# Performance work log

Measured on AMD Instinct MI355X. Metric: run time of the kernel, lower is better.

Reference implementation:

```python
import jax, jax.numpy as jnp
import numpy as np

C = 256      # d_model
H = 8        # nhead
DF = 1024    # dim_feedforward
LE = 2048    # ego tokens
LA = 2048    # other-agent tokens
N_MATCH = 1024


def setup_inputs() -> dict:
    key = jax.random.key(0)
    ks = jax.random.split(key, 16)
    def rn(k, shape, s=0.02):
        return jax.random.normal(k, shape, dtype=jnp.float32) * s
    inp = {}
    inp['x_ego'] = jax.random.normal(ks[0], (LE, C), dtype=jnp.float32)
    inp['x_agent'] = jax.random.normal(ks[1], (LA, C), dtype=jnp.float32)
    # query_fusion MLP(2C -> C -> C -> C), torch Linear weight is (out, in)
    inp['Wf1'] = rn(ks[2], (C, 2 * C)); inp['bf1'] = jnp.zeros((C,), jnp.float32)
    inp['Wf2'] = rn(ks[3], (C, C));     inp['bf2'] = jnp.zeros((C,), jnp.float32)
    inp['Wf3'] = rn(ks[4], (C, C));     inp['bf3'] = jnp.zeros((C,), jnp.float32)
    # nn.MultiheadAttention packed in-proj and out-proj
    inp['Wqkv'] = rn(ks[5], (3 * C, C)); inp['bqkv'] = jnp.zeros((3 * C,), jnp.float32)
    inp['Wo'] = rn(ks[6], (C, C));       inp['bo'] = jnp.zeros((C,), jnp.float32)
    # FFN
    inp['W1'] = rn(ks[7], (DF, C)); inp['b1'] = jnp.zeros((DF,), jnp.float32)
    inp['W2'] = rn(ks[8], (C, DF)); inp['b2'] = jnp.zeros((C,), jnp.float32)
    # LayerNorms
    inp['g1'] = jnp.ones((C,), jnp.float32); inp['be1'] = jnp.zeros((C,), jnp.float32)
    inp['g2'] = jnp.ones((C,), jnp.float32); inp['be2'] = jnp.zeros((C,), jnp.float32)
    # unique 1D positions: first N_MATCH agent positions overlap ego, rest don't
    inp['pos_ego'] = jnp.arange(LE, dtype=jnp.int32)
    pa = np.concatenate([np.arange(N_MATCH), np.arange(LA - N_MATCH) + 10_000_000])
    inp['pos_agent'] = jnp.asarray(pa, dtype=jnp.int32)
    inp['n_remain'] = LA - N_MATCH  # static python int
    return inp


def _ln(t, g, b):
    m = t.mean(-1, keepdims=True)
    v = t.var(-1, keepdims=True)
    return (t - m) / jnp.sqrt(v + 1e-5) * g + b


def reference(x_ego, x_agent, Wf1, bf1, Wf2, bf2, Wf3, bf3, Wqkv, bqkv, Wo, bo,
              W1, b1, W2, b2, g1, be1, g2, be2, pos_ego, pos_agent, n_remain):
    # ---- position-keyed grouping / fuse (replaces the host-side dict loop) ----
    eq = pos_agent[:, None] == pos_ego[None, :]          # [La, Le]
    matched_e = eq.any(axis=0)                           # ego token has same-pos agent token
    agent_for_ego = jnp.argmax(eq, axis=0)               # [Le] matching agent index (valid where matched)
    fused_in = jnp.concatenate([x_ego, x_agent[agent_for_ego]], axis=-1)  # [Le, 2C]
    h = jax.nn.relu(fused_in @ Wf1.T + bf1)
    h = jax.nn.relu(h @ Wf2.T + bf2)
    fused = h @ Wf3.T + bf3                              # query_fusion MLP output [Le, C]
    ego_out = jnp.where(matched_e[:, None], fused, x_ego)
    # agent tokens with no ego match, in original agent order (fixed count n_remain)
    remain_idx = jnp.nonzero(~eq.any(axis=1), size=n_remain)[0]
    q = jnp.concatenate([ego_out, x_agent[remain_idx]], axis=0)[None]  # (1, Lq, C)
    kv = jnp.concatenate([x_ego, x_agent], axis=0)[None]               # (1, Lk, C)
    # ---- MultiheadAttention (batch_first, eval: dropout off) ----
    Wq, Wk, Wv = jnp.split(Wqkv, 3, axis=0)
    bq, bk, bv = jnp.split(bqkv, 3, axis=0)
    dh = C // H
    def heads(t, W, b):
        return (t @ W.T + b).reshape(1, -1, H, dh).transpose(0, 2, 1, 3)
    qh, kh, vh = heads(q, Wq, bq), heads(kv, Wk, bk), heads(kv, Wv, bv)
    scores = jnp.einsum('bhqd,bhkd->bhqk', qh, kh) / (float(dh) ** 0.5)
    attn = jax.nn.softmax(scores, axis=-1)
    o = jnp.einsum('bhqk,bhkd->bhqd', attn, vh).transpose(0, 2, 1, 3).reshape(1, -1, C)
    o = o @ Wo.T + bo
    # ---- residual + norm1 + FFN + residual + norm2 ----
    yq = _ln(q + o, g1, be1)
    ff = jax.nn.relu(yq @ W1.T + b1) @ W2.T + b2
    return _ln(yq + ff, g2, be2)
```

## Files before the change

### kernel.cpp

```cpp
#include <hip/hip_runtime.h>


#define LE 2048
#define LA 2048
#define CDIM 256
#define HN 8
#define DH 32
#define DFF 1024
#define NREM 1024
#define LQC 3072
#define LKC 4096
#define KSPLIT 8
#define NIT (LKC / KSPLIT / 64)

typedef unsigned short u16;
typedef unsigned int u32;
typedef __attribute__((ext_vector_type(8))) short bf16x8;
typedef __attribute__((ext_vector_type(8))) _Float16 f16x8;
typedef __attribute__((ext_vector_type(4))) float f32x4;

#define MFMA __builtin_amdgcn_mfma_f32_16x16x32_bf16

__device__ __forceinline__ u32 pk_bf16(float a, float b) {
    u32 ua = (__builtin_bit_cast(u32, a) + 0x8000u) >> 16;
    u32 ub = (__builtin_bit_cast(u32, b) + 0x8000u) >> 16;
    return ua | (ub << 16);
}
__device__ __forceinline__ u16 bf16_1(float a) {
    return (u16)((__builtin_bit_cast(u32, a) + 0x8000u) >> 16);
}
__device__ __forceinline__ float fast_exp2(float x) {
    return __builtin_amdgcn_exp2f(x);
}
__device__ __forceinline__ bf16x8 ld_pack8(const float* p) {
    float4 f0 = *(const float4*)p;
    float4 f1 = *(const float4*)(p + 4);
    union { u32 u[4]; bf16x8 v; } o;
    o.u[0] = pk_bf16(f0.x, f0.y); o.u[1] = pk_bf16(f0.z, f0.w);
    o.u[2] = pk_bf16(f1.x, f1.y); o.u[3] = pk_bf16(f1.z, f1.w);
    return o.v;
}

struct WPtrs { const float* p[7]; };
__constant__ __device__ const int woff[8] = {0, 131072, 196608, 262144,
                                             458752, 524288, 786432, 1048576};

__global__ __launch_bounds__(1024) void k_prep(const int* __restrict__ pos_ego,
                                               const int* __restrict__ pos_agent,
                                               int* __restrict__ afe,
                                               int* __restrict__ matched,
                                               int* __restrict__ remain,
                                               const float* __restrict__ x_ego,
                                               const float* __restrict__ x_agent,
                                               WPtrs wp, u16* __restrict__ wb,
                                               u16* __restrict__ kv_b) {
    const int b = blockIdx.x;
    const int t = threadIdx.x;
    if (b == 0) {
        __shared__ int keyA[4096], valA[4096], keyE[4096];
        __shared__ int unm[2048];
#pragma unroll
        for (int i = 0; i < 4; ++i) { keyA[t + i * 1024] = -1; keyE[t + i * 1024] = -1; }
        __syncthreads();
#pragma unroll
        for (int i = 0; i < 2; ++i) {
            int a = t + i * 1024;
            int p = pos_agent[a];
            u32 h = ((u32)p * 2654435761u) >> 20;
            while (true) {
                int prev = atomicCAS(&keyA[h], -1, p);
                if (prev == -1) { valA[h] = a; break; }
                h = (h + 1) & 4095;
            }
// ... 43 lines not shown
            __syncthreads();
            valA[t] += v;
            __syncthreads();
        }
        int pos = valA[t] - cnt;
        if (f0 && pos < NREM) remain[pos] = 2 * t;
        if (f1 && pos + f0 < NREM) remain[pos + f0] = 2 * t + 1;
    } else if (b <= 128) {
        int g = ((b - 1) * 1024 + t) * 8;
        int s = 0;
#pragma unroll
        for (int i = 1; i < 7; ++i) s += (g >= woff[i]);
        const float* src = wp.p[s] + (g - woff[s]);
        float4 f0 = *(const float4*)(src);
        float4 f1 = *(const float4*)(src + 4);
        uint4 o;
        o.x = pk_bf16(f0.x, f0.y); o.y = pk_bf16(f0.z, f0.w);
        o.z = pk_bf16(f1.x, f1.y); o.w = pk_bf16(f1.z, f1.w);
        *(uint4*)(wb + g) = o;
    } else {
        int tt = (b - 129) * 1024 + t;
        int j = tt >> 5, c8 = tt & 31;
        const float* src = (j < LE) ? (x_ego + (size_t)j * CDIM)
                                    : (x_agent + (size_t)(j - LE) * CDIM);
        float4 f0 = *(const float4*)(src + c8 * 8);
        float4 f1 = *(const float4*)(src + c8 * 8 + 4);
        uint4 o;
        o.x = pk_bf16(f0.x, f0.y); o.y = pk_bf16(f0.z, f0.w);
        o.z = pk_bf16(f1.x, f1.y); o.w = pk_bf16(f1.z, f1.w);
        *(uint4*)(kv_b + (size_t)j * CDIM + c8 * 8) = o;
    }
}

__global__ __launch_bounds__(256) void k_fmlp(const float* __restrict__ x_ego,
                                              const float* __restrict__ x_agent,
                                              const int* __restrict__ afe,
                                              const int* __restrict__ matched,
                                              const int* __restrict__ remain,
                                              const u16* __restrict__ Wf1_b,
                                              const u16* __restrict__ Wf2_b,
                                              const u16* __restrict__ Wf3_b,
                                              const float* __restrict__ bf1,
                                              const float* __restrict__ bf2,
                                              const float* __restrict__ bf3,
                                              float* __restrict__ qbuf,
                                              u16* __restrict__ qbuf_b) {
    const int blk = blockIdx.x;
    const int tid = threadIdx.x;
    if (blk >= 128) {
        int rb = (blk - 128) * 64 + (tid >> 2);
        int row = LE + rb;
        int col = (tid & 3) * 64;
        int idx = remain[rb];
        idx = min(max(idx, 0), LA - 1);
        const float* src = x_agent + (size_t)idx * CDIM + col;
        float* dq = qbuf + (size_t)row * CDIM + col;
        u16* db = qbuf_b + (size_t)row * CDIM + col;
#pragma unroll
        for (int i = 0; i < 16; ++i) {
            float4 v = *(const float4*)(src + i * 4);
            *(float4*)(dq + i * 4) = v;
            *(uint2*)(db + i * 4) = make_uint2(pk_bf16(v.x, v.y), pk_bf16(v.z, v.w));
        }
        return;
    }
    __shared__ u16 h1[16 * 256];
    __shared__ u16 h2[16 * 256];
    const int w = tid >> 6, lane = tid & 63, quad = lane >> 4, qi = lane & 15;
    const int R0 = blk * 16;
    const int rg = R0 + qi;
    {
        const float* pe = x_ego + (size_t)rg * CDIM + quad * 8;
        const float* pg = x_agent + (size_t)afe[rg] * CDIM + quad * 8;
        f32x4 acc[4] = {};
        const u16* pb = Wf1_b + (size_t)(w * 64 + qi) * 512 + quad * 8;
#pragma unroll
        for (int kk = 0; kk < 256; kk += 32) {
            bf16x8 a = ld_pack8(pe + kk);
#pragma unroll
            for (int j = 0; j < 4; ++j) {
                bf16x8 bfr = *(const bf16x8*)(pb + (size_t)j * 16 * 512 + kk);
                acc[j] = MFMA(a, bfr, acc[j], 0, 0, 0);
            }
        }
#pragma unroll
        for (int kk = 0; kk < 256; kk += 32) {
            bf16x8 a = ld_pack8(pg + kk);
#pragma unroll
            for (int j = 0; j < 4; ++j) {
                bf16x8 bfr = *(const bf16x8*)(pb + (size_t)j * 16 * 512 + 256 + kk);
                acc[j] = MFMA(a, bfr, acc[j], 0, 0, 0);
            }
        }
#pragma unroll
        for (int j = 0; j < 4; ++j) {
            int col = w * 64 + j * 16 + qi;
            float bs = bf1[col];
#pragma unroll
            for (int r = 0; r < 4; ++r) {
                int row = quad * 4 + r;
                float v = fmaxf(acc[j][r] + bs, 0.f);
                int byte = (row * 512 + col * 2) ^ ((row & 7) << 4);
                *(u16*)((char*)h1 + byte) = bf16_1(v);
            }
        }
    }
    __syncthreads();
    {
        f32x4 acc[4] = {};
        const u16* pb = Wf2_b + (size_t)(w * 64 + qi) * 256 + quad * 8;
#pragma unroll
        for (int kk = 0; kk < 256; kk += 32) {
            int byte = (qi * 512 + (kk + quad * 8) * 2) ^ ((qi & 7) << 4);
            bf16x8 a = *(const bf16x8*)((char*)h1 + byte);
#pragma unroll
            for (int j = 0; j < 4; ++j) {
                bf16x8 bfr = *(const bf16x8*)(pb + (size_t)j * 16 * 256 + kk);
                acc[j] = MFMA(a, bfr, acc[j], 0, 0, 0);
            }
        }
#pragma unroll
        for (int j = 0; j < 4; ++j) {
            int col = w * 64 + j * 16 + qi;
            float bs = bf2[col];
#pragma unroll
            for (int r = 0; r < 4; ++r) {
                int row = quad * 4 + r;
                float v = fmaxf(acc[j][r] + bs, 0.f);
                int byte = (row * 512 + col * 2) ^ ((row & 7) << 4);
                *(u16*)((char*)h2 + byte) = bf16_1(v);
            }
        }
    }
    __syncthreads();
    {
        f32x4 acc[4] = {};
        const u16* pb = Wf3_b + (size_t)(w * 64 + qi) * 256 + quad * 8;
#pragma unroll
        for (int kk = 0; kk < 256; kk += 32) {
            int byte = (qi * 512 + (kk + quad * 8) * 2) ^ ((qi & 7) << 4);
            bf16x8 a = *(const bf16x8*)((char*)h2 + byte);
#pragma unroll
            for (int j = 0; j < 4; ++j) {
                bf16x8 bfr = *(const bf16x8*)(pb + (size_t)j * 16 * 256 + kk);
                acc[j] = MFMA(a, bfr, acc[j], 0, 0, 0);
            }
        }
        int m[4];
#pragma unroll
        for (int r = 0; r < 4; ++r) m[r] = matched[R0 + quad * 4 + r];
#pragma unroll
        for (int j = 0; j < 4; ++j) {
            int col = w * 64 + j * 16 + qi;
            float bs = bf3[col];
#pragma unroll
            for (int r = 0; r < 4; ++r) {
                int row = R0 + quad * 4 + r;
                float v = acc[j][r] + bs;
                if (!m[r]) v = x_ego[(size_t)row * CDIM + col];
                qbuf[(size_t)row * CDIM + col] = v;
                qbuf_b[(size_t)row * CDIM + col] = bf16_1(v);
            }
        }
    }
}

__global__ __launch_bounds__(256) void k_qkv(const u16* __restrict__ qbuf_b,
                                             const u16* __restrict__ kv_b,
                                             const u16* __restrict__ Wq,
                                             const u16* __restrict__ Wkv,
                                             const float* __restrict__ bqkv,
                                             u16* __restrict__ qb,
                                             u16* __restrict__ kbp,
                                             u16* __restrict__ vtb,
                                             float qscale) {
    int b;
    {
        int p = blockIdx.x;
        int c = p & 7, s = p >> 3;
        b = c * 88 + s;
    }
    const u16 *A, *B;
    const float* bias;
    int bm, bn, mode;
    if (b < 192) {
        A = qbuf_b; B = Wq; bias = bqkv;
        bm = (b >> 2) * 64; bn = (b & 3) * 64; mode = 0;
    } else {
        int c = b - 192;
        A = kv_b; B = Wkv; bias = bqkv + 256;
        bm = (c >> 3) * 64; bn = (c & 7) * 64; mode = 1;
    }
    const int tid = threadIdx.x;
    const int w = tid >> 6, lane = tid & 63;
    const int quad = lane >> 4, qi = lane & 15;
    const int wm = w >> 1, wn = w & 1;
    const int K = 256;

    const u16* pa0 = A + (size_t)(bm + wm * 32 + qi) * K + quad * 8;
// ... 136 lines not shown
        bf16x8 pa0 = *(bf16x8*)&pb[rd0];
        bf16x8 pa1 = *(bf16x8*)&pb[rd1];

        bf16x8 v00 = *(const bf16x8*)&Vt[buf][v00o];
        bf16x8 v01 = *(const bf16x8*)&Vt[buf][v01o];
        bf16x8 v10 = *(const bf16x8*)&Vt[buf][v00o + 16 * 64];
        bf16x8 v11 = *(const bf16x8*)&Vt[buf][v01o + 16 * 64];
        O0 = MFMA(pa0, v00, O0, 0, 0, 0);
        O0 = MFMA(pa1, v01, O0, 0, 0, 0);
        O1 = MFMA(pa0, v10, O1, 0, 0, 0);
        O1 = MFMA(pa1, v11, O1, 0, 0, 0);

        if (more) {
            *(bf16x8*)&Kt[buf ^ 1][kdst] = knext;
            *(bf16x8*)&Vt[buf ^ 1][vdst] = vnext;
        }
        buf ^= 1;
    }

    lsum += __shfl_xor(lsum, 16, 64);
    lsum += __shfl_xor(lsum, 32, 64);

    int pbase = (h * KSPLIT + ks) * LQC + q0;
    if (quad == 0) Pl[pbase + qi] = lsum;
#pragma unroll
    for (int r = 0; r < 4; ++r) {
        int q = quad * 4 + r;
        u16* pa = Pacc + (size_t)(pbase + q) * 32;
        pa[qi] = __builtin_bit_cast(u16, (_Float16)O0[r]);
        pa[16 + qi] = __builtin_bit_cast(u16, (_Float16)O1[r]);
    }
}

__global__ __launch_bounds__(256) void k_oln(const float* __restrict__ Pl,
                                             const u16* __restrict__ Pacc,
                                             const u16* __restrict__ Wo_b,
                                             const float* __restrict__ bo,
                                             const float* __restrict__ qbuf,
                                             const float* __restrict__ g1,
                                             const float* __restrict__ be1,
                                             float* __restrict__ yq,
                                             u16* __restrict__ yq_b) {
    __shared__ u16 At[16 * 256];
    __shared__ float red[16][4][2];
    const int tid = threadIdx.x;
    const int R0 = blockIdx.x * 16;
    {
        int row = tid >> 4, cg = tid & 15;
        int h = cg >> 1, dh = (cg & 1) * 16;
        int r = R0 + row;
        float L = 0.f;
        float o[16] = {};
#pragma unroll
        for (int ks = 0; ks < 8; ++ks) {
            size_t pidx = (size_t)(h * 8 + ks) * LQC + r;
            L += Pl[pidx];
            const u16* pa = Pacc + pidx * 32 + dh;
            f16x8 v0 = *(const f16x8*)(pa);
            f16x8 v1 = *(const f16x8*)(pa + 8);
#pragma unroll
            for (int i = 0; i < 8; ++i) {
                o[i] += (float)v0[i];
                o[8 + i] += (float)v1[i];
            }
        }
        float invL = 1.0f / L;
        int cb = h * 32 + dh;
#pragma unroll
        for (int i = 0; i < 8; ++i) {
            int c0 = cb + 2 * i;
            u32 pk = pk_bf16(o[2 * i] * invL, o[2 * i + 1] * invL);
            int byte = (row * 512 + c0 * 2) ^ ((row & 7) << 4);
            *(u32*)((char*)At + byte) = pk;
        }
    }
    __syncthreads();
    const int w = tid >> 6, lane = tid & 63, quad = lane >> 4, qi = lane & 15;
    f32x4 acc[4] = {};
    const u16* pb = Wo_b + (size_t)(w * 64 + qi) * 256 + quad * 8;
#pragma unroll
    for (int kk = 0; kk < 256; kk += 32) {
        int byte = (qi * 512 + (kk + quad * 8) * 2) ^ ((qi & 7) << 4);
        bf16x8 a = *(const bf16x8*)((char*)At + byte);
#pragma unroll
        for (int j = 0; j < 4; ++j) {
            bf16x8 bfr = *(const bf16x8*)(pb + (size_t)j * 16 * 256 + kk);
            acc[j] = MFMA(a, bfr, acc[j], 0, 0, 0);
        }
    }
    float v[4][4], s[4] = {}, sq[4] = {};
#pragma unroll
    for (int j = 0; j < 4; ++j) {
        int col = w * 64 + j * 16 + qi;
        float bs = bo[col];
#pragma unroll
        for (int r = 0; r < 4; ++r) {
            int row = R0 + quad * 4 + r;
            float x = acc[j][r] + bs + qbuf[(size_t)row * CDIM + col];
            v[j][r] = x; s[r] += x; sq[r] += x * x;
        }
    }
#pragma unroll
    for (int off = 1; off < 16; off <<= 1) {
#pragma unroll
        for (int r = 0; r < 4; ++r) {
            s[r] += __shfl_xor(s[r], off, 64);
            sq[r] += __shfl_xor(sq[r], off, 64);
        }
    }
    if (qi == 0) {
#pragma unroll
        for (int r = 0; r < 4; ++r) {
            red[quad * 4 + r][w][0] = s[r];
            red[quad * 4 + r][w][1] = sq[r];
        }
    }
    __syncthreads();
    float mean[4], rstd[4];
#pragma unroll
    for (int r = 0; r < 4; ++r) {
        int rl = quad * 4 + r;
        float st = red[rl][0][0] + red[rl][1][0] + red[rl][2][0] + red[rl][3][0];
        float sqt = red[rl][0][1] + red[rl][1][1] + red[rl][2][1] + red[rl][3][1];
        mean[r] = st * (1.f / 256.f);
        float var = sqt * (1.f / 256.f) - mean[r] * mean[r];
        rstd[r] = rsqrtf(var + 1e-5f);
    }
#pragma unroll
    for (int j = 0; j < 4; ++j) {
        int col = w * 64 + j * 16 + qi;
        float gg = g1[col], bb = be1[col];
#pragma unroll
        for (int r = 0; r < 4; ++r) {
            int row = R0 + quad * 4 + r;
            float o = (v[j][r] - mean[r]) * rstd[r] * gg + bb;
            yq[(size_t)row * CDIM + col] = o;
            yq_b[(size_t)row * CDIM + col] = bf16_1(o);
        }
    }
}

__global__ __launch_bounds__(256) void k_ffn(const u16* __restrict__ yq_b,
                                             const float* __restrict__ yq,
                                             const u16* __restrict__ W1_b,
                                             const float* __restrict__ b1,
                                             const u16* __restrict__ W2_b,
                                             const float* __restrict__ b2,
                                             const float* __restrict__ g2,
                                             const float* __restrict__ be2,
                                             float* __restrict__ out) {
    __shared__ u16 hT[16 * 1024];
    __shared__ float red[16][4][2];
    const int tid = threadIdx.x;
    const int w = tid >> 6, lane = tid & 63, quad = lane >> 4, qi = lane & 15;
    const int R0 = blockIdx.x * 16;
    {
        const u16* pa = yq_b + (size_t)(R0 + qi) * 256 + quad * 8;
        f32x4 acc[16] = {};
        const u16* pb = W1_b + (size_t)(w * 256 + qi) * 256 + quad * 8;
#pragma unroll
        for (int kk = 0; kk < 256; kk += 32) {
            bf16x8 a = *(const bf16x8*)(pa + kk);
#pragma unroll
            for (int j = 0; j < 16; ++j) {
                bf16x8 bfr = *(const bf16x8*)(pb + (size_t)j * 16 * 256 + kk);
                acc[j] = MFMA(a, bfr, acc[j], 0, 0, 0);
            }
        }
#pragma unroll
        for (int j = 0; j < 16; ++j) {
            int col = w * 256 + j * 16 + qi;
            float bs = b1[col];
#pragma unroll
            for (int r = 0; r < 4; ++r) {
                int row = quad * 4 + r;
                float v = fmaxf(acc[j][r] + bs, 0.f);
                int byte = (row * 2048 + col * 2) ^ ((row & 7) << 4);
                *(u16*)((char*)hT + byte) = bf16_1(v);
            }
        }
    }
    __syncthreads();
    f32x4 acc[4] = {};
    const u16* pb = W2_b + (size_t)(w * 64 + qi) * 1024 + quad * 8;
#pragma unroll 4
    for (int kk = 0; kk < 1024; kk += 32) {
        int byte = (qi * 2048 + (kk + quad * 8) * 2) ^ ((qi & 7) << 4);
        bf16x8 a = *(const bf16x8*)((char*)hT + byte);
#pragma unroll
        for (int j = 0; j < 4; ++j) {
            bf16x8 bfr = *(const bf16x8*)(pb + (size_t)j * 16 * 1024 + kk);
            acc[j] = MFMA(a, bfr, acc[j], 0, 0, 0);
        }
    }
    float v[4][4], s[4] = {}, sq[4] = {};
#pragma unroll
    for (int j = 0; j < 4; ++j) {
        int col = w * 64 + j * 16 + qi;
        float bs = b2[col];
#pragma unroll
        for (int r = 0; r < 4; ++r) {
            int row = R0 + quad * 4 + r;
            float x = acc[j][r] + bs + yq[(size_t)row * CDIM + col];
            v[j][r] = x; s[r] += x; sq[r] += x * x;
        }
    }
#pragma unroll
    for (int off = 1; off < 16; off <<= 1) {
#pragma unroll
        for (int r = 0; r < 4; ++r) {
            s[r] += __shfl_xor(s[r], off, 64);
            sq[r] += __shfl_xor(sq[r], off, 64);
        }
    }
    if (qi == 0) {
#pragma unroll
        for (int r = 0; r < 4; ++r) {
            red[quad * 4 + r][w][0] = s[r];
            red[quad * 4 + r][w][1] = sq[r];
        }
    }
    __syncthreads();
    float mean[4], rstd[4];
#pragma unroll
    for (int r = 0; r < 4; ++r) {
        int rl = quad * 4 + r;
        float st = red[rl][0][0] + red[rl][1][0] + red[rl][2][0] + red[rl][3][0];
        float sqt = red[rl][0][1] + red[rl][1][1] + red[rl][2][1] + red[rl][3][1];
        mean[r] = st * (1.f / 256.f);
        float var = sqt * (1.f / 256.f) - mean[r] * mean[r];
        rstd[r] = rsqrtf(var + 1e-5f);
    }
#pragma unroll
    for (int j = 0; j < 4; ++j) {
        int col = w * 64 + j * 16 + qi;
        float gg = g2[col], bb = be2[col];
#pragma unroll
        for (int r = 0; r < 4; ++r) {
            int row = R0 + quad * 4 + r;
            out[(size_t)row * CDIM + col] = (v[j][r] - mean[r]) * rstd[r] * gg + bb;
        }
    }
}

extern "C" void kernel_launch(void* const* d_in, const int* in_sizes, int n_in,
                              void* d_out, int out_size, void* d_ws, size_t ws_size,
                              hipStream_t stream) {
    const float* x_ego = (const float*)d_in[0];
    const float* x_agent = (const float*)d_in[1];
    const float* Wf1 = (const float*)d_in[2];
    const float* bf1 = (const float*)d_in[3];
    const float* Wf2 = (const float*)d_in[4];
    const float* bf2 = (const float*)d_in[5];
    const float* Wf3 = (const float*)d_in[6];
    const float* bf3 = (const float*)d_in[7];
    const float* Wqkv = (const float*)d_in[8];
    const float* bqkv = (const float*)d_in[9];
    const float* Wo = (const float*)d_in[10];
    const float* bo = (const float*)d_in[11];
    const float* W1 = (const float*)d_in[12];
    const float* b1 = (const float*)d_in[13];
    const float* W2 = (const float*)d_in[14];
    const float* b2 = (const float*)d_in[15];
    const float* g1 = (const float*)d_in[16];
    const float* be1 = (const float*)d_in[17];
    const float* g2 = (const float*)d_in[18];
    const float* be2 = (const float*)d_in[19];
    const int* pos_ego = (const int*)d_in[20];
    const int* pos_agent = (const int*)d_in[21];

    float* ws = (float*)d_ws;
    size_t o = 0;
    float* qbuf = ws + o; o += 786432;
    float* yq = ws + o; o += 786432;
    float* Pl = ws + o; o += HN * KSPLIT * LQC;
    u16* Pacc = (u16*)(ws + o); o += (size_t)HN * KSPLIT * LQC * 16;
    u16* wb = (u16*)(ws + o); o += 524288;
    u16* qbuf_b = (u16*)(ws + o); o += 393216;
    u16* kv_b = (u16*)(ws + o); o += 524288;
    u16* qb = (u16*)(ws + o); o += 393216;
    u16* kb = (u16*)(ws + o); o += 524288;
    u16* vtb = (u16*)(ws + o); o += 524288;
    u16* yq_b = (u16*)(ws + o); o += 393216;
    int* afe = (int*)(ws + o);
    int* matched = afe + LE;
    int* remain = matched + LE;

    const u16* Wf1_b = wb + 0;
    const u16* Wf2_b = wb + 131072;
    const u16* Wf3_b = wb + 196608;
    const u16* Wq_b = wb + 262144;
    const u16* Wkv_b = wb + 327680;
    const u16* Wo_b = wb + 458752;
    const u16* W1_b = wb + 524288;
    const u16* W2_b = wb + 786432;

    WPtrs wp;
    wp.p[0] = Wf1; wp.p[1] = Wf2; wp.p[2] = Wf3; wp.p[3] = Wqkv;
    wp.p[4] = Wo; wp.p[5] = W1; wp.p[6] = W2;

    k_prep<<<257, 1024, 0, stream>>>(pos_ego, pos_agent, afe, matched, remain,
                                     x_ego, x_agent, wp, wb, kv_b);

    const float qscale = 0.17677669529663687f * 1.4426950408889634f;

    k_fmlp<<<144, 256, 0, stream>>>(x_ego, x_agent, afe, matched, remain,
                                    Wf1_b, Wf2_b, Wf3_b, bf1, bf2, bf3,
                                    qbuf, qbuf_b);

    k_qkv<<<704, 256, 0, stream>>>(qbuf_b, kv_b, Wq_b, Wkv_b, bqkv, qb, kb, vtb, qscale);

    attn_mfma<<<dim3(LQC / 64, HN, KSPLIT), 256, 0, stream>>>(qb, kb, vtb, Pl, Pacc);

    k_oln<<<LQC / 16, 256, 0, stream>>>(Pl, Pacc, Wo_b, bo, qbuf, g1, be1, yq, yq_b);

    k_ffn<<<LQC / 16, 256, 0, stream>>>(yq_b, yq, W1_b, b1, W2_b, b2, g2, be2,
                                        (float*)d_out);
}
```

Measured before the change: 223.0 us.

## Repartition row-wise MLP/LN kernels into 8-row, 1024-thread blocks

The fused-MLP, out-proj+LayerNorm and FFN kernels switch from 16-row blocks of 4 waves to 8-row blocks of 16 waves, each wave owning a narrower column slice. This doubles the grid and spreads the GEMM work over more waves so more CUs stay busy on these small-M stages. The cost is that half of each 16x16 MFMA tile is wasted, because only 8 rows are valid and rows are duplicated across quads, so weights are re-read by twice as many blocks. The LayerNorm reductions now combine partials from 16 waves.

```diff
diff --git a/kernel.cpp b/kernel.cpp
--- a/kernel.cpp
+++ b/kernel.cpp
@@ -16,7 +16,7 @@
 typedef unsigned short u16;
 typedef unsigned int u32;
 typedef __attribute__((ext_vector_type(8))) short bf16x8;
-typedef __attribute__((ext_vector_type(8))) _Float16 f16x8;
+typedef __attribute__((ext_vector_type(2))) _Float16 f16x2;
 typedef __attribute__((ext_vector_type(4))) float f32x4;
 
 #define MFMA __builtin_amdgcn_mfma_f32_16x16x32_bf16
@@ -148,134 +148,106 @@
     }
 }
 
-__global__ __launch_bounds__(256) void k_fmlp(const float* __restrict__ x_ego,
-                                              const float* __restrict__ x_agent,
-                                              const int* __restrict__ afe,
-                                              const int* __restrict__ matched,
-                                              const int* __restrict__ remain,
-                                              const u16* __restrict__ Wf1_b,
-                                              const u16* __restrict__ Wf2_b,
-                                              const u16* __restrict__ Wf3_b,
-                                              const float* __restrict__ bf1,
-                                              const float* __restrict__ bf2,
-                                              const float* __restrict__ bf3,
-                                              float* __restrict__ qbuf,
-                                              u16* __restrict__ qbuf_b) {
+__global__ __launch_bounds__(1024) void k_fmlp(const float* __restrict__ x_ego,
+                                               const float* __restrict__ x_agent,
+                                               const int* __restrict__ afe,
+                                               const int* __restrict__ matched,
+                                               const int* __restrict__ remain,
+                                               const u16* __restrict__ Wf1_b,
+                                               const u16* __restrict__ Wf2_b,
+                                               const u16* __restrict__ Wf3_b,
+                                               const float* __restrict__ bf1,
+                                               const float* __restrict__ bf2,
+                                               const float* __restrict__ bf3,
+                                               float* __restrict__ qbuf,
+                                               u16* __restrict__ qbuf_b) {
     const int blk = blockIdx.x;
     const int tid = threadIdx.x;
-    if (blk >= 128) {
-        int rb = (blk - 128) * 64 + (tid >> 2);
+    if (blk >= 256) {
+        int rb = (blk - 256) * 128 + (tid >> 3);
         int row = LE + rb;
-        int col = (tid & 3) * 64;
+        int col = (tid & 7) * 32;
         int idx = remain[rb];
         idx = min(max(idx, 0), LA - 1);
         const float* src = x_agent + (size_t)idx * CDIM + col;
         float* dq = qbuf + (size_t)row * CDIM + col;
         u16* db = qbuf_b + (size_t)row * CDIM + col;
 #pragma unroll
-        for (int i = 0; i < 16; ++i) {
+        for (int i = 0; i < 8; ++i) {
             float4 v = *(const float4*)(src + i * 4);
             *(float4*)(dq + i * 4) = v;
             *(uint2*)(db + i * 4) = make_uint2(pk_bf16(v.x, v.y), pk_bf16(v.z, v.w));
         }
         return;
     }
-    __shared__ u16 h1[16 * 256];
-    __shared__ u16 h2[16 * 256];
+    __shared__ u16 h1[8 * 256];
+    __shared__ u16 h2[8 * 256];
     const int w = tid >> 6, lane = tid & 63, quad = lane >> 4, qi = lane & 15;
-    const int R0 = blk * 16;
-    const int rg = R0 + qi;
+    const int R0 = blk * 8;
+    const int ar = qi & 7;
+    const int col = w * 16 + qi;
     {
-        const float* pe = x_ego + (size_t)rg * CDIM + quad * 8;
-        const float* pg = x_agent + (size_t)afe[rg] * CDIM + quad * 8;
-        f32x4 acc[4] = {};
-        const u16* pb = Wf1_b + (size_t)(w * 64 + qi) * 512 + quad * 8;
-#pragma unroll
-        for (int kk = 0; kk < 256; kk += 32) {
-            bf16x8 a = ld_pack8(pe + kk);
-#pragma unroll
-            for (int j = 0; j < 4; ++j) {
-                bf16x8 bfr = *(const bf16x8*)(pb + (size_t)j * 16 * 512 + kk);
-                acc[j] = MFMA(a, bfr, acc[j], 0, 0, 0);
-            }
-        }
-#pragma unroll
-        for (int kk = 0; kk < 256; kk += 32) {
-            bf16x8 a = ld_pack8(pg + kk);
-#pragma unroll
-            for (int j = 0; j < 4; ++j) {
-                bf16x8 bfr = *(const bf16x8*)(pb + (size_t)j * 16 * 512 + 256 + kk);
-                acc[j] = MFMA(a, bfr, acc[j], 0, 0, 0);
-            }
-        }
-#pragma unroll
-        for (int j = 0; j < 4; ++j) {
-            int col = w * 64 + j * 16 + qi;
+        const float* pe = x_ego + (size_t)(R0 + ar) * CDIM + quad * 8;
+        const float* pg = x_agent + (size_t)afe[R0 + ar] * CDIM + quad * 8;
+        f32x4 acc = {};
+        const u16* pb = Wf1_b + (size_t)col * 512 + quad * 8;
+#pragma unroll
+        for (int kk = 0; kk < 256; kk += 32)
+            acc = MFMA(ld_pack8(pe + kk), *(const bf16x8*)(pb + kk), acc, 0, 0, 0);
+#pragma unroll
+        for (int kk = 0; kk < 256; kk += 32)
+            acc = MFMA(ld_pack8(pg + kk), *(const bf16x8*)(pb + 256 + kk), acc, 0, 0, 0);
+        if (quad < 2) {
             float bs = bf1[col];
 #pragma unroll
             for (int r = 0; r < 4; ++r) {
                 int row = quad * 4 + r;
-                float v = fmaxf(acc[j][r] + bs, 0.f);
-                int byte = (row * 512 + col * 2) ^ ((row & 7) << 4);
-                *(u16*)((char*)h1 + byte) = bf16_1(v);
+                float vv = fmaxf(acc[r] + bs, 0.f);
+                int byte = (row * 512 + col * 2) ^ (row << 4);
+                *(u16*)((char*)h1 + byte) = bf16_1(vv);
             }
         }
     }
     __syncthreads();
     {
-        f32x4 acc[4] = {};
-        const u16* pb = Wf2_b + (size_t)(w * 64 + qi) * 256 + quad * 8;
+        f32x4 acc = {};
+        const u16* pb = Wf2_b + (size_t)col * 256 + quad * 8;
 #pragma unroll
         for (int kk = 0; kk < 256; kk += 32) {
-            int byte = (qi * 512 + (kk + quad * 8) * 2) ^ ((qi & 7) << 4);
-            bf16x8 a = *(const bf16x8*)((char*)h1 + byte);
-#pragma unroll
-            for (int j = 0; j < 4; ++j) {
-                bf16x8 bfr = *(const bf16x8*)(pb + (size_t)j * 16 * 256 + kk);
-                acc[j] = MFMA(a, bfr, acc[j], 0, 0, 0);
-            }
-        }
-#pragma unroll
-        for (int j = 0; j < 4; ++j) {
-            int col = w * 64 + j * 16 + qi;
+            int byte = (ar * 512 + (kk + quad * 8) * 2) ^ (ar << 4);
+            acc = MFMA(*(const bf16x8*)((char*)h1 + byte),
+                       *(const bf16x8*)(pb + kk), acc, 0, 0, 0);
+        }
+        if (quad < 2) {
             float bs = bf2[col];
 #pragma unroll
             for (int r = 0; r < 4; ++r) {
                 int row = quad * 4 + r;
-                float v = fmaxf(acc[j][r] + bs, 0.f);
-                int byte = (row * 512 + col * 2) ^ ((row & 7) << 4);
-                *(u16*)((char*)h2 + byte) = bf16_1(v);
+                float vv = fmaxf(acc[r] + bs, 0.f);
+                int byte = (row * 512 + col * 2) ^ (row << 4);
+                *(u16*)((char*)h2 + byte) = bf16_1(vv);
             }
         }
     }
     __syncthreads();
     {
-        f32x4 acc[4] = {};
-        const u16* pb = Wf3_b + (size_t)(w * 64 + qi) * 256 + quad * 8;
+        f32x4 acc = {};
+        const u16* pb = Wf3_b + (size_t)col * 256 + quad * 8;
 #pragma unroll
         for (int kk = 0; kk < 256; kk += 32) {
-            int byte = (qi * 512 + (kk + quad * 8) * 2) ^ ((qi & 7) << 4);
-            bf16x8 a = *(const bf16x8*)((char*)h2 + byte);
-#pragma unroll
-            for (int j = 0; j < 4; ++j) {
-                bf16x8 bfr = *(const bf16x8*)(pb + (size_t)j * 16 * 256 + kk);
-                acc[j] = MFMA(a, bfr, acc[j], 0, 0, 0);
-            }
-        }
-        int m[4];
-#pragma unroll
-        for (int r = 0; r < 4; ++r) m[r] = matched[R0 + quad * 4 + r];
-#pragma unroll
-        for (int j = 0; j < 4; ++j) {
-            int col = w * 64 + j * 16 + qi;
+            int byte = (ar * 512 + (kk + quad * 8) * 2) ^ (ar << 4);
+            acc = MFMA(*(const bf16x8*)((char*)h2 + byte),
+                       *(const bf16x8*)(pb + kk), acc, 0, 0, 0);
+        }
+        if (quad < 2) {
             float bs = bf3[col];
 #pragma unroll
             for (int r = 0; r < 4; ++r) {
                 int row = R0 + quad * 4 + r;
-                float v = acc[j][r] + bs;
-                if (!m[r]) v = x_ego[(size_t)row * CDIM + col];
-                qbuf[(size_t)row * CDIM + col] = v;
-                qbuf_b[(size_t)row * CDIM + col] = bf16_1(v);
+                float vv = acc[r] + bs;
+                if (!matched[row]) vv = x_ego[(size_t)row * CDIM + col];
+                qbuf[(size_t)row * CDIM + col] = vv;
+                qbuf_b[(size_t)row * CDIM + col] = bf16_1(vv);
             }
         }
     }
@@ -483,213 +455,179 @@
     }
 }
 
-__global__ __launch_bounds__(256) void k_oln(const float* __restrict__ Pl,
-                                             const u16* __restrict__ Pacc,
-                                             const u16* __restrict__ Wo_b,
-                                             const float* __restrict__ bo,
-                                             const float* __restrict__ qbuf,
-                                             const float* __restrict__ g1,
-                                             const float* __restrict__ be1,
-                                             float* __restrict__ yq,
-                                             u16* __restrict__ yq_b) {
-    __shared__ u16 At[16 * 256];
-    __shared__ float red[16][4][2];
+__global__ __launch_bounds__(1024) void k_oln(const float* __restrict__ Pl,
+                                              const u16* __restrict__ Pacc,
+                                              const u16* __restrict__ Wo_b,
+                                              const float* __restrict__ bo,
+                                              const float* __restrict__ qbuf,
+                                              const float* __restrict__ g1,
+                                              const float* __restrict__ be1,
+                                              float* __restrict__ yq,
+                                              u16* __restrict__ yq_b) {
+    __shared__ u16 At[8 * 256];
+    __shared__ float red[8][16][2];
     const int tid = threadIdx.x;
-    const int R0 = blockIdx.x * 16;
+    const int R0 = blockIdx.x * 8;
     {
-        int row = tid >> 4, cg = tid & 15;
-        int h = cg >> 1, dh = (cg & 1) * 16;
+        int row = tid >> 7, cg = tid & 127;
+        int h = cg >> 4, dh2 = (cg & 15) * 2;
         int r = R0 + row;
-        float L = 0.f;
-        float o[16] = {};
+        float L = 0.f, o0 = 0.f, o1 = 0.f;
 #pragma unroll
         for (int ks = 0; ks < 8; ++ks) {
             size_t pidx = (size_t)(h * 8 + ks) * LQC + r;
             L += Pl[pidx];
-            const u16* pa = Pacc + pidx * 32 + dh;
-            f16x8 v0 = *(const f16x8*)(pa);
-            f16x8 v1 = *(const f16x8*)(pa + 8);
-#pragma unroll
-            for (int i = 0; i < 8; ++i) {
-                o[i] += (float)v0[i];
-                o[8 + i] += (float)v1[i];
-            }
+            f16x2 v = *(const f16x2*)(Pacc + pidx * 32 + dh2);
+            o0 += (float)v[0]; o1 += (float)v[1];
         }
         float invL = 1.0f / L;
-        int cb = h * 32 + dh;
-#pragma unroll
-        for (int i = 0; i < 8; ++i) {
-            int c0 = cb + 2 * i;
-            u32 pk = pk_bf16(o[2 * i] * invL, o[2 * i + 1] * invL);
-            int byte = (row * 512 + c0 * 2) ^ ((row & 7) << 4);
-            *(u32*)((char*)At + byte) = pk;
-        }
+        int col = h * 32 + dh2;
+        int byte = (row * 512 + col * 2) ^ (row << 4);
+        *(u32*)((char*)At + byte) = pk_bf16(o0 * invL, o1 * invL);
     }
     __syncthreads();
     const int w = tid >> 6, lane = tid & 63, quad = lane >> 4, qi = lane & 15;
-    f32x4 acc[4] = {};
-    const u16* pb = Wo_b + (size_t)(w * 64 + qi) * 256 + quad * 8;
+    const int ar = qi & 7;
+    const int col = w * 16 + qi;
+    f32x4 acc = {};
+    const u16* pb = Wo_b + (size_t)col * 256 + quad * 8;
 #pragma unroll
     for (int kk = 0; kk < 256; kk += 32) {
-        int byte = (qi * 512 + (kk + quad * 8) * 2) ^ ((qi & 7) << 4);
-        bf16x8 a = *(const bf16x8*)((char*)At + byte);
-#pragma unroll
-        for (int j = 0; j < 4; ++j) {
-            bf16x8 bfr = *(const bf16x8*)(pb + (size_t)j * 16 * 256 + kk);
-            acc[j] = MFMA(a, bfr, acc[j], 0, 0, 0);
-        }
-    }
-    float v[4][4], s[4] = {}, sq[4] = {};
-#pragma unroll
-    for (int j = 0; j < 4; ++j) {
-        int col = w * 64 + j * 16 + qi;
-        float bs = bo[col];
-#pragma unroll
-        for (int r = 0; r < 4; ++r) {
-            int row = R0 + quad * 4 + r;
-            float x = acc[j][r] + bs + qbuf[(size_t)row * CDIM + col];
-            v[j][r] = x; s[r] += x; sq[r] += x * x;
-        }
-    }
-#pragma unroll
-    for (int off = 1; off < 16; off <<= 1) {
+        int byte = (ar * 512 + (kk + quad * 8) * 2) ^ (ar << 4);
+        acc = MFMA(*(const bf16x8*)((char*)At + byte),
+                   *(const bf16x8*)(pb + kk), acc, 0, 0, 0);
+    }
+    float v[4], s[4], sq[4];
+    float bs = bo[col];
+#pragma unroll
+    for (int r = 0; r < 4; ++r) {
+        int row = R0 + (quad & 1) * 4 + r;
+        float x = acc[r] + bs + qbuf[(size_t)row * CDIM + col];
+        v[r] = x; s[r] = x; sq[r] = x * x;
+    }
+#pragma unroll
+    for (int off = 1; off < 16; off <<= 1)
 #pragma unroll
         for (int r = 0; r < 4; ++r) {
             s[r] += __shfl_xor(s[r], off, 64);
             sq[r] += __shfl_xor(sq[r], off, 64);
         }
-    }
-    if (qi == 0) {
+    if (qi == 0 && quad < 2)
 #pragma unroll
         for (int r = 0; r < 4; ++r) {
             red[quad * 4 + r][w][0] = s[r];
             red[quad * 4 + r][w][1] = sq[r];
         }
-    }
     __syncthreads();
-    float mean[4], rstd[4];
-#pragma unroll
-    for (int r = 0; r < 4; ++r) {
-        int rl = quad * 4 + r;
-        float st = red[rl][0][0] + red[rl][1][0] + red[rl][2][0] + red[rl][3][0];
-        float sqt = red[rl][0][1] + red[rl][1][1] + red[rl][2][1] + red[rl][3][1];
-        mean[r] = st * (1.f / 256.f);
-        float var = sqt * (1.f / 256.f) - mean[r] * mean[r];
-        rstd[r] = rsqrtf(var + 1e-5f);
-    }
-#pragma unroll
-    for (int j = 0; j < 4; ++j) {
-        int col = w * 64 + j * 16 + qi;
+    if (quad < 2) {
         float gg = g1[col], bb = be1[col];
 #pragma unroll
         for (int r = 0; r < 4; ++r) {
-            int row = R0 + quad * 4 + r;
-            float o = (v[j][r] - mean[r]) * rstd[r] * gg + bb;
+            int rl = quad * 4 + r;
+            float st = 0.f, sqt = 0.f;
+#pragma unroll
+            for (int ww = 0; ww < 16; ++ww) {
+                st += red[rl][ww][0]; sqt += red[rl][ww][1];
+            }
+            float mean = st * (1.f / 256.f);
+            float var = sqt * (1.f / 256.f) - mean * mean;
+            float rstd = rsqrtf(var + 1e-5f);
+            int row = R0 + rl;
+            float o = (v[r] - mean) * rstd * gg + bb;
             yq[(size_t)row * CDIM + col] = o;
             yq_b[(size_t)row * CDIM + col] = bf16_1(o);
         }
     }
 }
 
-__global__ __launch_bounds__(256) void k_ffn(const u16* __restrict__ yq_b,
-                                             const float* __restrict__ yq,
-                                             const u16* __restrict__ W1_b,
-                                             const float* __restrict__ b1,
-                                             const u16* __restrict__ W2_b,
-                                             const float* __restrict__ b2,
-                                             const float* __restrict__ g2,
-                                             const float* __restrict__ be2,
-                                             float* __restrict__ out) {
-    __shared__ u16 hT[16 * 1024];
-    __shared__ float red[16][4][2];
+__global__ __launch_bounds__(1024) void k_ffn(const u16* __restrict__ yq_b,
+                                              const float* __restrict__ yq,
+                                              const u16* __restrict__ W1_b,
+                                              const float* __restrict__ b1,
+                                              const u16* __restrict__ W2_b,
+                                              const float* __restrict__ b2,
+                                              const float* __restrict__ g2,
+                                              const float* __restrict__ be2,
+                                              float* __restrict__ out) {
+    __shared__ u16 hT[8 * 1024];
+    __shared__ float red[8][16][2];
     const int tid = threadIdx.x;
     const int w = tid >> 6, lane = tid & 63, quad = lane >> 4, qi = lane & 15;
-    const int R0 = blockIdx.x * 16;
+    const int R0 = blockIdx.x * 8;
+    const int ar = qi & 7;
     {
-        const u16* pa = yq_b + (size_t)(R0 + qi) * 256 + quad * 8;
-        f32x4 acc[16] = {};
-        const u16* pb = W1_b + (size_t)(w * 256 + qi) * 256 + quad * 8;
+        const u16* pa = yq_b + (size_t)(R0 + ar) * 256 + quad * 8;
+        f32x4 acc[4] = {};
+        const u16* pb = W1_b + (size_t)(w * 64 + qi) * 256 + quad * 8;
 #pragma unroll
         for (int kk = 0; kk < 256; kk += 32) {
             bf16x8 a = *(const bf16x8*)(pa + kk);
 #pragma unroll
-            for (int j = 0; j < 16; ++j) {
-                bf16x8 bfr = *(const bf16x8*)(pb + (size_t)j * 16 * 256 + kk);
-                acc[j] = MFMA(a, bfr, acc[j], 0, 0, 0);
-            }
-        }
-#pragma unroll
-        for (int j = 0; j < 16; ++j) {
-            int col = w * 256 + j * 16 + qi;
-            float bs = b1[col];
-#pragma unroll
-            for (int r = 0; r < 4; ++r) {
-                int row = quad * 4 + r;
-                float v = fmaxf(acc[j][r] + bs, 0.f);
-                int byte = (row * 2048 + col * 2) ^ ((row & 7) << 4);
-                *(u16*)((char*)hT + byte) = bf16_1(v);
-            }
-        }
+            for (int j = 0; j < 4; ++j)
+                acc[j] = MFMA(a, *(const bf16x8*)(pb + (size_t)j * 16 * 256 + kk),
+                              acc[j], 0, 0, 0);
+        }
+        if (quad < 2)
+#pragma unroll
+            for (int j = 0; j < 4; ++j) {
+                int col = w * 64 + j * 16 + qi;
+                float bs = b1[col];
+#pragma unroll
+                for (int r = 0; r < 4; ++r) {
+                    int row = quad * 4 + r;
+                    float vv = fmaxf(acc[j][r] + bs, 0.f);
+                    int byte = (row * 2048 + col * 2) ^ (row << 4);
+                    *(u16*)((char*)hT + byte) = bf16_1(vv);
+                }
+            }
     }
     __syncthreads();
-    f32x4 acc[4] = {};
-    const u16* pb = W2_b + (size_t)(w * 64 + qi) * 1024 + quad * 8;
+    const int col = w * 16 + qi;
+    f32x4 acc = {};
+    const u16* pb = W2_b + (size_t)col * 1024 + quad * 8;
 #pragma unroll 4
     for (int kk = 0; kk < 1024; kk += 32) {
-        int byte = (qi * 2048 + (kk + quad * 8) * 2) ^ ((qi & 7) << 4);
-        bf16x8 a = *(const bf16x8*)((char*)hT + byte);
-#pragma unroll
-        for (int j = 0; j < 4; ++j) {
-            bf16x8 bfr = *(const bf16x8*)(pb + (size_t)j * 16 * 1024 + kk);
-            acc[j] = MFMA(a, bfr, acc[j], 0, 0, 0);
-        }
-    }
-    float v[4][4], s[4] = {}, sq[4] = {};
-#pragma unroll
-    for (int j = 0; j < 4; ++j) {
-        int col = w * 64 + j * 16 + qi;
-        float bs = b2[col];
-#pragma unroll
-        for (int r = 0; r < 4; ++r) {
-            int row = R0 + quad * 4 + r;
-            float x = acc[j][r] + bs + yq[(size_t)row * CDIM + col];
-            v[j][r] = x; s[r] += x; sq[r] += x * x;
-        }
-    }
-#pragma unroll
-    for (int off = 1; off < 16; off <<= 1) {
+        int byte = (ar * 2048 + (kk + quad * 8) * 2) ^ (ar << 4);
+        acc = MFMA(*(const bf16x8*)((char*)hT + byte),
+                   *(const bf16x8*)(pb + kk), acc, 0, 0, 0);
+    }
+    float v[4], s[4], sq[4];
+    float bs = b2[col];
+#pragma unroll
+    for (int r = 0; r < 4; ++r) {
+        int row = R0 + (quad & 1) * 4 + r;
+        float x = acc[r] + bs + yq[(size_t)row * CDIM + col];
+        v[r] = x; s[r] = x; sq[r] = x * x;
+    }
+#pragma unroll
+    for (int off = 1; off < 16; off <<= 1)
 #pragma unroll
         for (int r = 0; r < 4; ++r) {
             s[r] += __shfl_xor(s[r], off, 64);
             sq[r] += __shfl_xor(sq[r], off, 64);
         }
-    }
-    if (qi == 0) {
+    if (qi == 0 && quad < 2)
 #pragma unroll
         for (int r = 0; r < 4; ++r) {
             red[quad * 4 + r][w][0] = s[r];
             red[quad * 4 + r][w][1] = sq[r];
         }
-    }
     __syncthreads();
-    float mean[4], rstd[4];
-#pragma unroll
-    for (int r = 0; r < 4; ++r) {
-        int rl = quad * 4 + r;
-        float st = red[rl][0][0] + red[rl][1][0] + red[rl][2][0] + red[rl][3][0];
-        float sqt = red[rl][0][1] + red[rl][1][1] + red[rl][2][1] + red[rl][3][1];
-        mean[r] = st * (1.f / 256.f);
-        float var = sqt * (1.f / 256.f) - mean[r] * mean[r];
-        rstd[r] = rsqrtf(var + 1e-5f);
-    }
-#pragma unroll
-    for (int j = 0; j < 4; ++j) {
-        int col = w * 64 + j * 16 + qi;
+    if (quad < 2) {
         float gg = g2[col], bb = be2[col];
 #pragma unroll
         for (int r = 0; r < 4; ++r) {
-            int row = R0 + quad * 4 + r;
-            out[(size_t)row * CDIM + col] = (v[j][r] - mean[r]) * rstd[r] * gg + bb;
+            int rl = quad * 4 + r;
+            float st = 0.f, sqt = 0.f;
+#pragma unroll
+            for (int ww = 0; ww < 16; ++ww) {
+                st += red[rl][ww][0]; sqt += red[rl][ww][1];
+            }
+            float mean = st * (1.f / 256.f);
+            float var = sqt * (1.f / 256.f) - mean * mean;
+            float rstd = rsqrtf(var + 1e-5f);
+            int row = R0 + rl;
+            out[(size_t)row * CDIM + col] = (v[r] - mean) * rstd * gg + bb;
         }
     }
 }
@@ -755,16 +693,16 @@
 
     const float qscale = 0.17677669529663687f * 1.4426950408889634f;
 
-    k_fmlp<<<144, 256, 0, stream>>>(x_ego, x_agent, afe, matched, remain,
-                                    Wf1_b, Wf2_b, Wf3_b, bf1, bf2, bf3,
-                                    qbuf, qbuf_b);
+    k_fmlp<<<264, 1024, 0, stream>>>(x_ego, x_agent, afe, matched, remain,
+                                     Wf1_b, Wf2_b, Wf3_b, bf1, bf2, bf3,
+                                     qbuf, qbuf_b);
 
     k_qkv<<<704, 256, 0, stream>>>(qbuf_b, kv_b, Wq_b, Wkv_b, bqkv, qb, kb, vtb, qscale);
 
     attn_mfma<<<dim3(LQC / 64, HN, KSPLIT), 256, 0, stream>>>(qb, kb, vtb, Pl, Pacc);
 
-    k_oln<<<LQC / 16, 256, 0, stream>>>(Pl, Pacc, Wo_b, bo, qbuf, g1, be1, yq, yq_b);
-
-    k_ffn<<<LQC / 16, 256, 0, stream>>>(yq_b, yq, W1_b, b1, W2_b, b2, g2, be2,
+    k_oln<<<LQC / 8, 1024, 0, stream>>>(Pl, Pacc, Wo_b, bo, qbuf, g1, be1, yq, yq_b);
+
+    k_ffn<<<LQC / 8, 1024, 0, stream>>>(yq_b, yq, W1_b, b1, W2_b, b2, g2, be2,
                                         (float*)d_out);
 }
```

After: 266.7 us. 19.6% more time.

## Split fused FFN kernel into separate GEMM, GEMM and LayerNorm kernels

Applied to the files above, without the earlier changes.

Replaces the single fused FFN kernel, which kept the ReLU hidden tile in LDS and fused the residual LayerNorm, with three kernels: a tiled bf16 GEMM for W1 with ReLU that writes the hidden activations to global memory, a second GEMM for W2 that writes fp32 output, and a standalone residual+LayerNorm kernel. The intent is higher parallelism, with grids of 768 and 384 blocks instead of 192, plus XCD-aware tile mapping. In exchange it adds two kernel launches and global round trips for the 3072x1024 bf16 hidden tensor and the fp32 FFN output.

```diff
diff --git a/kernel.cpp b/kernel.cpp
--- a/kernel.cpp
+++ b/kernel.cpp
@@ -16,6 +16,7 @@
 typedef unsigned short u16;
 typedef unsigned int u32;
 typedef __attribute__((ext_vector_type(8))) short bf16x8;
+typedef __attribute__((ext_vector_type(2))) _Float16 f16x2;
 typedef __attribute__((ext_vector_type(8))) _Float16 f16x8;
 typedef __attribute__((ext_vector_type(4))) float f32x4;
 
@@ -39,6 +40,16 @@
     o.u[0] = pk_bf16(f0.x, f0.y); o.u[1] = pk_bf16(f0.z, f0.w);
     o.u[2] = pk_bf16(f1.x, f1.y); o.u[3] = pk_bf16(f1.z, f1.w);
     return o.v;
+}
+
+__device__ __forceinline__ void xcd_tile(int& bm, int& bn) {
+    int gx = gridDim.x;
+    int tot = gx * gridDim.y;
+    int p = blockIdx.y * gx + blockIdx.x;
+    int l = p;
+    if (!(tot & 7)) { int c = p & 7, s = p >> 3; l = c * (tot >> 3) + s; }
+    bm = (l / gx) * 64;
+    bn = (l % gx) * 64;
 }
 
 struct WPtrs { const float* p[7]; };
@@ -281,6 +292,111 @@
     }
 }
 
+template <int EPI, bool RELU>
+__global__ __launch_bounds__(256) void gemm_bf16(const u16* __restrict__ A,
+                                                 const u16* __restrict__ B,
+                                                 const float* __restrict__ bias,
+                                                 void* __restrict__ C,
+                                                 int M, int N, int K) {
+    const int tid = threadIdx.x;
+    const int w = tid >> 6, lane = tid & 63;
+    const int quad = lane >> 4, qi = lane & 15;
+    const int wm = w >> 1, wn = w & 1;
+    int bm, bn;
+    xcd_tile(bm, bn);
+
+    const u16* pa0 = A + (size_t)(bm + wm * 32 + qi) * K + quad * 8;
+    const u16* pa1 = pa0 + (size_t)16 * K;
+    const u16* pb0 = B + (size_t)(bn + wn * 32 + qi) * K + quad * 8;
+    const u16* pb1 = pb0 + (size_t)16 * K;
+
+    f32x4 acc00 = {0.f, 0.f, 0.f, 0.f}, acc01 = {0.f, 0.f, 0.f, 0.f};
+    f32x4 acc10 = {0.f, 0.f, 0.f, 0.f}, acc11 = {0.f, 0.f, 0.f, 0.f};
+
+#pragma unroll 4
+    for (int k = 0; k < K; k += 32) {
+        bf16x8 a0 = *(const bf16x8*)(pa0 + k);
+        bf16x8 a1 = *(const bf16x8*)(pa1 + k);
+        bf16x8 b0 = *(const bf16x8*)(pb0 + k);
+        bf16x8 b1 = *(const bf16x8*)(pb1 + k);
+        acc00 = MFMA(a0, b0, acc00, 0, 0, 0);
+        acc01 = MFMA(a0, b1, acc01, 0, 0, 0);
+        acc10 = MFMA(a1, b0, acc10, 0, 0, 0);
+        acc11 = MFMA(a1, b1, acc11, 0, 0, 0);
+    }
+
+#pragma unroll
+    for (int i = 0; i < 2; ++i) {
+#pragma unroll
+        for (int j = 0; j < 2; ++j) {
+            f32x4 acc = (i == 0) ? (j == 0 ? acc00 : acc01) : (j == 0 ? acc10 : acc11);
+            int n = bn + wn * 32 + j * 16 + qi;
+            int mbase = bm + wm * 32 + i * 16 + quad * 4;
+            float bs = bias[n];
+            float v[4];
+#pragma unroll
+            for (int r = 0; r < 4; ++r) {
+                float x = acc[r] + bs;
+                if (RELU) x = fmaxf(x, 0.f);
+                v[r] = x;
+            }
+            if (EPI == 0) {
+                float* Cf = (float*)C;
+#pragma unroll
+                for (int r = 0; r < 4; ++r) Cf[(size_t)(mbase + r) * N + n] = v[r];
+            } else {
+                u16* Cb = (u16*)C;
+#pragma unroll
+                for (int r = 0; r < 4; ++r) Cb[(size_t)(mbase + r) * N + n] = bf16_1(v[r]);
+            }
+        }
+    }
+}
+
+__global__ __launch_bounds__(256) void gemm32(const u16* __restrict__ A,
+                                              const u16* __restrict__ B,
+                                              const float* __restrict__ bias,
+                                              float* __restrict__ C,
+                                              int M, int N, int K) {
+    const int tid = threadIdx.x;
+    const int w = tid >> 6, lane = tid & 63;
+    const int quad = lane >> 4, qi = lane & 15;
+    const int rh = w >> 1, ch = w & 1;
+    int bm, bn;
+    {
+        int gx = gridDim.x;
+        int tot = gx * gridDim.y;
+        int p = blockIdx.y * gx + blockIdx.x;
+        int l = p;
+        if (!(tot & 7)) { int c = p & 7, s = p >> 3; l = c * (tot >> 3) + s; }
+        bm = (l / gx) * 32;
+        bn = (l % gx) * 64;
+    }
+    const u16* pa = A + (size_t)(bm + rh * 16 + qi) * K + quad * 8;
+    const u16* pb0 = B + (size_t)(bn + ch * 32 + qi) * K + quad * 8;
+    const u16* pb1 = pb0 + (size_t)16 * K;
+
+    f32x4 acc0 = {0.f, 0.f, 0.f, 0.f}, acc1 = {0.f, 0.f, 0.f, 0.f};
+#pragma unroll 8
+    for (int k = 0; k < K; k += 32) {
+        bf16x8 a = *(const bf16x8*)(pa + k);
+        bf16x8 b0 = *(const bf16x8*)(pb0 + k);
+        bf16x8 b1 = *(const bf16x8*)(pb1 + k);
+        acc0 = MFMA(a, b0, acc0, 0, 0, 0);
+        acc1 = MFMA(a, b1, acc1, 0, 0, 0);
+    }
+#pragma unroll
+    for (int j = 0; j < 2; ++j) {
+        f32x4 acc = j == 0 ? acc0 : acc1;
+        int n = bn + ch * 32 + j * 16 + qi;
+        int mbase = bm + rh * 16 + quad * 4;
+        float bs = bias[n];
+#pragma unroll
+        for (int r = 0; r < 4; ++r)
+            C[(size_t)(mbase + r) * N + n] = acc[r] + bs;
+    }
+}
+
 __global__ __launch_bounds__(256) void k_qkv(const u16* __restrict__ qbuf_b,
                                              const u16* __restrict__ kv_b,
                                              const u16* __restrict__ Wq,
@@ -591,106 +707,42 @@
     }
 }
 
-__global__ __launch_bounds__(256) void k_ffn(const u16* __restrict__ yq_b,
-                                             const float* __restrict__ yq,
-                                             const u16* __restrict__ W1_b,
-                                             const float* __restrict__ b1,
-                                             const u16* __restrict__ W2_b,
-                                             const float* __restrict__ b2,
-                                             const float* __restrict__ g2,
-                                             const float* __restrict__ be2,
-                                             float* __restrict__ out) {
-    __shared__ u16 hT[16 * 1024];
-    __shared__ float red[16][4][2];
-    const int tid = threadIdx.x;
-    const int w = tid >> 6, lane = tid & 63, quad = lane >> 4, qi = lane & 15;
-    const int R0 = blockIdx.x * 16;
-    {
-        const u16* pa = yq_b + (size_t)(R0 + qi) * 256 + quad * 8;
-        f32x4 acc[16] = {};
-        const u16* pb = W1_b + (size_t)(w * 256 + qi) * 256 + quad * 8;
-#pragma unroll
-        for (int kk = 0; kk < 256; kk += 32) {
-            bf16x8 a = *(const bf16x8*)(pa + kk);
-#pragma unroll
-            for (int j = 0; j < 16; ++j) {
-                bf16x8 bfr = *(const bf16x8*)(pb + (size_t)j * 16 * 256 + kk);
-                acc[j] = MFMA(a, bfr, acc[j], 0, 0, 0);
-            }
-        }
-#pragma unroll
-        for (int j = 0; j < 16; ++j) {
-            int col = w * 256 + j * 16 + qi;
-            float bs = b1[col];
-#pragma unroll
-            for (int r = 0; r < 4; ++r) {
-                int row = quad * 4 + r;
-                float v = fmaxf(acc[j][r] + bs, 0.f);
-                int byte = (row * 2048 + col * 2) ^ ((row & 7) << 4);
-                *(u16*)((char*)hT + byte) = bf16_1(v);
-            }
-        }
-    }
-    __syncthreads();
-    f32x4 acc[4] = {};
-    const u16* pb = W2_b + (size_t)(w * 64 + qi) * 1024 + quad * 8;
-#pragma unroll 4
-    for (int kk = 0; kk < 1024; kk += 32) {
-        int byte = (qi * 2048 + (kk + quad * 8) * 2) ^ ((qi & 7) << 4);
-        bf16x8 a = *(const bf16x8*)((char*)hT + byte);
-#pragma unroll
-        for (int j = 0; j < 4; ++j) {
-            bf16x8 bfr = *(const bf16x8*)(pb + (size_t)j * 16 * 1024 + kk);
-            acc[j] = MFMA(a, bfr, acc[j], 0, 0, 0);
-        }
-    }
-    float v[4][4], s[4] = {}, sq[4] = {};
-#pragma unroll
-    for (int j = 0; j < 4; ++j) {
-        int col = w * 64 + j * 16 + qi;
-        float bs = b2[col];
-#pragma unroll
-        for (int r = 0; r < 4; ++r) {
-            int row = R0 + quad * 4 + r;
-            float x = acc[j][r] + bs + yq[(size_t)row * CDIM + col];
-            v[j][r] = x; s[r] += x; sq[r] += x * x;
-        }
-    }
-#pragma unroll
-    for (int off = 1; off < 16; off <<= 1) {
-#pragma unroll
-        for (int r = 0; r < 4; ++r) {
-            s[r] += __shfl_xor(s[r], off, 64);
-            sq[r] += __shfl_xor(sq[r], off, 64);
-        }
-    }
-    if (qi == 0) {
-#pragma unroll
-        for (int r = 0; r < 4; ++r) {
-            red[quad * 4 + r][w][0] = s[r];
-            red[quad * 4 + r][w][1] = sq[r];
-        }
-    }
-    __syncthreads();
-    float mean[4], rstd[4];
-#pragma unroll
-    for (int r = 0; r < 4; ++r) {
-        int rl = quad * 4 + r;
-        float st = red[rl][0][0] + red[rl][1][0] + red[rl][2][0] + red[rl][3][0];
-        float sqt = red[rl][0][1] + red[rl][1][1] + red[rl][2][1] + red[rl][3][1];
-        mean[r] = st * (1.f / 256.f);
-        float var = sqt * (1.f / 256.f) - mean[r] * mean[r];
-        rstd[r] = rsqrtf(var + 1e-5f);
-    }
-#pragma unroll
-    for (int j = 0; j < 4; ++j) {
-        int col = w * 64 + j * 16 + qi;
-        float gg = g2[col], bb = be2[col];
-#pragma unroll
-        for (int r = 0; r < 4; ++r) {
-            int row = R0 + quad * 4 + r;
-            out[(size_t)row * CDIM + col] = (v[j][r] - mean[r]) * rstd[r] * gg + bb;
-        }
+template <bool EMIT_BF16>
+__global__ __launch_bounds__(256) void ln_kernel(const float* __restrict__ X,
+                                                 const float* __restrict__ R,
+                                                 const float* __restrict__ g,
+                                                 const float* __restrict__ b,
+                                                 float* __restrict__ out,
+                                                 u16* __restrict__ out_b) {
+    int lane = threadIdx.x & 63;
+    int row = blockIdx.x * 4 + (threadIdx.x >> 6);
+    const float* x = X + (size_t)row * CDIM;
+    const float* r = R + (size_t)row * CDIM;
+    float4 xv = *(const float4*)(x + lane * 4);
+    float4 rv = *(const float4*)(r + lane * 4);
+    float v[4] = {xv.x + rv.x, xv.y + rv.y, xv.z + rv.z, xv.w + rv.w};
+    float s = v[0] + v[1] + v[2] + v[3];
+    float sq = v[0] * v[0] + v[1] * v[1] + v[2] * v[2] + v[3] * v[3];
+#pragma unroll
+    for (int off = 32; off >= 1; off >>= 1) {
+        s += __shfl_xor(s, off, 64);
+        sq += __shfl_xor(sq, off, 64);
+    }
+    float mean = s * (1.f / 256.f);
+    float var = sq * (1.f / 256.f) - mean * mean;
+    float rstd = rsqrtf(var + 1e-5f);
+    float4 gv = *(const float4*)(g + lane * 4);
+    float4 bv = *(const float4*)(b + lane * 4);
+    float4 o = make_float4((v[0] - mean) * rstd * gv.x + bv.x,
+                           (v[1] - mean) * rstd * gv.y + bv.y,
+                           (v[2] - mean) * rstd * gv.z + bv.z,
+                           (v[3] - mean) * rstd * gv.w + bv.w);
+    *(float4*)(out + (size_t)row * CDIM + lane * 4) = o;
+    if (EMIT_BF16) {
+        uint2 ob;
+        ob.x = pk_bf16(o.x, o.y);
+        ob.y = pk_bf16(o.z, o.w);
+        *(uint2*)(out_b + (size_t)row * CDIM + lane * 4) = ob;
     }
 }
 
@@ -724,6 +776,7 @@
     size_t o = 0;
     float* qbuf = ws + o; o += 786432;
     float* yq = ws + o; o += 786432;
+    float* ff2 = ws + o; o += 786432;
     float* Pl = ws + o; o += HN * KSPLIT * LQC;
     u16* Pacc = (u16*)(ws + o); o += (size_t)HN * KSPLIT * LQC * 16;
     u16* wb = (u16*)(ws + o); o += 524288;
@@ -733,6 +786,7 @@
     u16* kb = (u16*)(ws + o); o += 524288;
     u16* vtb = (u16*)(ws + o); o += 524288;
     u16* yq_b = (u16*)(ws + o); o += 393216;
+    u16* ff1_b = (u16*)(ws + o); o += 1572864;
     int* afe = (int*)(ws + o);
     int* matched = afe + LE;
     int* remain = matched + LE;
@@ -765,6 +819,8 @@
 
     k_oln<<<LQC / 16, 256, 0, stream>>>(Pl, Pacc, Wo_b, bo, qbuf, g1, be1, yq, yq_b);
 
-    k_ffn<<<LQC / 16, 256, 0, stream>>>(yq_b, yq, W1_b, b1, W2_b, b2, g2, be2,
-                                        (float*)d_out);
-}
+    gemm_bf16<1, true><<<dim3(16, 48), 256, 0, stream>>>(yq_b, W1_b, b1, ff1_b,
+                                                         LQC, DFF, 256);
+    gemm32<<<dim3(4, 96), 256, 0, stream>>>(ff1_b, W2_b, b2, ff2, LQC, 256, DFF);
+    ln_kernel<false><<<LQC / 4, 256, 0, stream>>>(yq, ff2, g2, be2, (float*)d_out, nullptr);
+}
```

Result: faster. 216.0 us (-3.1%).
